# Kernel tuning notes

Hardware: AMD Instinct MI355X
Metric: run time of the kernel (lower is better)

The kernel has to match this reference:

```python
import jax, jax.numpy as jnp
import numpy as np


def _sobel_kernels(dtype):
    # kornia sobel order=1, normalized: divide by sum(|k|)=8
    gx = jnp.array([[-1., 0., 1.], [-2., 0., 2.], [-1., 0., 1.]], dtype=dtype) / 8.0
    gy = gx.T
    return jnp.stack([gx, gy])[:, None]  # (2, 1, 3, 3) OIHW


def _spatial_gradient(x):
    # x: (b, c, h, w) -> gx, gy each (b, c, h, w)
    b, c, h, w = x.shape
    xp = jnp.pad(x.reshape(b * c, 1, h, w), ((0, 0), (0, 0), (1, 1), (1, 1)), mode='edge')
    k = _sobel_kernels(x.dtype)
    out = jax.lax.conv_general_dilated(
        xp, k, window_strides=(1, 1), padding='VALID',
        dimension_numbers=('NCHW', 'OIHW', 'NCHW'))  # (b*c, 2, h, w)
    out = out.reshape(b, c, 2, h, w)
    return out[:, :, 0], out[:, :, 1]


def setup_inputs() -> dict:
    key = jax.random.key(0)
    x = jax.random.normal(key, (16, 3, 512, 512), dtype=jnp.float32)
    return {"x": x}


def reference(x):
    b, c, h, w = x.shape
    gx, gy = _spatial_gradient(x)  # (b, c, h, w) each
    if c == 3:
        mag_c = jnp.sqrt(gx * gx + gy * gy + 1e-9)  # per-channel magnitude
        # first-occurrence argmax over channels matches torch .max(dim) tie-break
        idx = jnp.argmax(mag_c, axis=1)  # (b, h, w)
        gxs = jnp.take_along_axis(gx, idx[:, None], axis=1)[:, 0]  # (b, h, w)
        gys = jnp.take_along_axis(gy, idx[:, None], axis=1)[:, 0]
    else:
        gxs, gys = gx, gy
    magnitude = jnp.sqrt(gxs * gxs + gys * gys + 1e-9)
    # clipped_div(gx, gy, 10.0)
    y_tr = jnp.where(gys == 0.0, jnp.asarray(1e-9, gys.dtype), gys)
    angle = jnp.clip(gxs / y_tr, -10.0, 10.0)
    return magnitude, angle
```

## Files before the change

### kernel.cpp

```cpp
#include <hip/hip_runtime.h>
#include <stdint.h>


constexpr int Hc = 512;
constexpr int Wc = 512;
constexpr int Cc = 3;
constexpr int RT = 4;
constexpr int TR = RT + 2;

__global__ __launch_bounds__(256, 4) void sobel_mag_angle_kernel(
    const float* __restrict__ x, float* __restrict__ out, int B) {
    __shared__ float lds[Cc * TR * Wc];

    int bid = blockIdx.x;
    int b  = bid >> 7;
    int h0 = (bid & 127) * RT;

    int t = threadIdx.x;
    int wave = t >> 6;
    int lane = t & 63;

    const float* xb = x + (size_t)b * (Cc * Hc * Wc);
#pragma unroll
    for (int s2 = 0; s2 < 9; ++s2) {
        int s = wave * 9 + s2;
        int ch = s / 12;
        int rr = (s % 12) >> 1;
        int half = s & 1;
        int srow = h0 + rr - 1;
        srow = srow < 0 ? 0 : (srow > Hc - 1 ? Hc - 1 : srow);
        const float* gp = xb + ((size_t)ch * Hc + srow) * Wc + half * 256 + lane * 4;
        float* lp = &lds[(ch * TR + rr) * Wc + half * 256];
        __builtin_amdgcn_global_load_lds(
            (const __attribute__((address_space(1))) void*)gp,
            (__attribute__((address_space(3))) void*)lp, 16, 0, 0);
    }
    asm volatile("s_waitcnt vmcnt(0)" ::: "memory");
    __syncthreads();

    int r = wave;
    int w0 = lane << 3;
    int wl = (w0 == 0) ? 0 : w0 - 1;
    int wr = (w0 + 8 < Wc) ? w0 + 8 : Wc - 1;

    float bm[8], bgx[8], bgy[8];
#pragma unroll
    for (int c = 0; c < Cc; ++c) {
        float row[3][10];
#pragma unroll
        for (int k = 0; k < 3; ++k) {
            const float* lrow = &lds[(c * TR + (r + k)) * Wc];
            float4 A  = *(const float4*)(lrow + w0);
            float4 Bv = *(const float4*)(lrow + w0 + 4);
            row[k][0] = lrow[wl];
            row[k][1] = A.x;  row[k][2] = A.y;  row[k][3] = A.z;  row[k][4] = A.w;
            row[k][5] = Bv.x; row[k][6] = Bv.y; row[k][7] = Bv.z; row[k][8] = Bv.w;
            row[k][9] = lrow[wr];
        }
#pragma unroll
        for (int i = 0; i < 8; ++i) {
            float t0 = row[0][i + 2] - row[0][i];
            float t1 = row[1][i + 2] - row[1][i];
            float t2 = row[2][i + 2] - row[2][i];
            float gx = 0.125f * (t0 + t2) + 0.25f * t1;
            float u0 = row[2][i]     - row[0][i];
            float u1 = row[2][i + 1] - row[0][i + 1];
            float u2 = row[2][i + 2] - row[0][i + 2];
            float gy = 0.125f * (u0 + u2) + 0.25f * u1;
            float m = __builtin_amdgcn_sqrtf(gx * gx + gy * gy + 1e-9f);
            if (c == 0) {
                bm[i] = m; bgx[i] = gx; bgy[i] = gy;
            } else {
                bool gt = m > bm[i];
                bm[i]  = gt ? m  : bm[i];
                bgx[i] = gt ? gx : bgx[i];
                bgy[i] = gt ? gy : bgy[i];
            }
        }
    }

    float mo[8], ao[8];
#pragma unroll
    for (int i = 0; i < 8; ++i) {
        mo[i] = bm[i];
        float yt = (bgy[i] == 0.0f) ? 1e-9f : bgy[i];
        float a = bgx[i] * __builtin_amdgcn_rcpf(yt);
        ao[i] = fminf(fmaxf(a, -10.0f), 10.0f);
    }

    size_t npix = (size_t)B * (Hc * Wc);
    size_t obase = ((size_t)b * Hc + (h0 + r)) * Wc;
    float* po = out + obase;
    *(float4*)(po + w0)            = make_float4(mo[0], mo[1], mo[2], mo[3]);
    *(float4*)(po + w0 + 4)        = make_float4(mo[4], mo[5], mo[6], mo[7]);
    *(float4*)(po + npix + w0)     = make_float4(ao[0], ao[1], ao[2], ao[3]);
    *(float4*)(po + npix + w0 + 4) = make_float4(ao[4], ao[5], ao[6], ao[7]);
}

extern "C" void kernel_launch(void* const* d_in, const int* in_sizes, int n_in,
                              void* d_out, int out_size, void* d_ws, size_t ws_size,
                              hipStream_t stream) {
    const float* x = (const float*)d_in[0];
    float* out = (float*)d_out;
    int B = in_sizes[0] / (Cc * Hc * Wc);
    int blocks = B * (Hc / RT);
    sobel_mag_angle_kernel<<<blocks, 256, 0, stream>>>(x, out, B);
}
```

Baseline: 96.31 us.

## Make blocks persistent over row strips with triple-buffered async LDS loads

Each block now walks 32 rows in 8 iterations instead of handling one 4-row tile. A 3-slot LDS ring is filled with global_load_lds two stages ahead, and counted vmcnt waits let loads overlap compute. Halo rows are no longer reloaded per tile, and the horizontal halo columns now come from wave shuffles instead of extra LDS reads. The grid shrinks to 256 blocks and LDS use per block grows, which lowers occupancy and may leave too little parallelism to hide memory latency on a GPU with many CUs.

```diff
diff --git a/kernel.cpp b/kernel.cpp
--- a/kernel.cpp
+++ b/kernel.cpp
@@ -6,95 +6,117 @@
 constexpr int Wc = 512;
 constexpr int Cc = 3;
 constexpr int RT = 4;
-constexpr int TR = RT + 2;
+constexpr int ITERS = 8;
+constexpr int SLOTS = 3;
+constexpr int TILE_F = Cc * RT * Wc;
 
-__global__ __launch_bounds__(256, 4) void sobel_mag_angle_kernel(
+__global__ __launch_bounds__(256, 1) void sobel_mag_angle_kernel(
     const float* __restrict__ x, float* __restrict__ out, int B) {
-    __shared__ float lds[Cc * TR * Wc];
+    __shared__ float lds[SLOTS * TILE_F];
 
     int bid = blockIdx.x;
-    int b  = bid >> 7;
-    int h0 = (bid & 127) * RT;
+    int b = bid >> 4;
+    int bstart = (bid & 15) << 5;
 
     int t = threadIdx.x;
     int wave = t >> 6;
     int lane = t & 63;
+    int w0 = lane << 3;
+    bool l0 = (lane == 0), l63 = (lane == 63);
 
     const float* xb = x + (size_t)b * (Cc * Hc * Wc);
+
+    auto stage = [&](int j) {
+        int slot = j % SLOTS;
 #pragma unroll
-    for (int s2 = 0; s2 < 9; ++s2) {
-        int s = wave * 9 + s2;
-        int ch = s / 12;
-        int rr = (s % 12) >> 1;
-        int half = s & 1;
-        int srow = h0 + rr - 1;
-        srow = srow < 0 ? 0 : (srow > Hc - 1 ? Hc - 1 : srow);
-        const float* gp = xb + ((size_t)ch * Hc + srow) * Wc + half * 256 + lane * 4;
-        float* lp = &lds[(ch * TR + rr) * Wc + half * 256];
-        __builtin_amdgcn_global_load_lds(
-            (const __attribute__((address_space(1))) void*)gp,
-            (__attribute__((address_space(3))) void*)lp, 16, 0, 0);
-    }
-    asm volatile("s_waitcnt vmcnt(0)" ::: "memory");
-    __syncthreads();
+        for (int s2 = 0; s2 < 6; ++s2) {
+            int s = wave * 6 + s2;
+            int c = s >> 3;
+            int k = (s >> 1) & 3;
+            int half = s & 1;
+            int g = bstart - 1 + (j << 2) + k;
+            g = g < 0 ? 0 : (g > Hc - 1 ? Hc - 1 : g);
+            const float* gp = xb + ((size_t)c * Hc + g) * Wc + half * 256 + lane * 4;
+            float* lp = &lds[slot * TILE_F + (c * RT + k) * Wc + half * 256];
+            __builtin_amdgcn_global_load_lds(
+                (const __attribute__((address_space(1))) void*)gp,
+                (__attribute__((address_space(3))) void*)lp, 16, 0, 0);
+        }
+    };
 
-    int r = wave;
-    int w0 = lane << 3;
-    int wl = (w0 == 0) ? 0 : w0 - 1;
-    int wr = (w0 + 8 < Wc) ? w0 + 8 : Wc - 1;
+    stage(0);
+    stage(1);
 
-    float bm[8], bgx[8], bgy[8];
+    size_t npix = (size_t)B * (Hc * Wc);
+
+    for (int i = 0; i < ITERS; ++i) {
+        stage(i + 2);
+        asm volatile("s_waitcnt vmcnt(6)" ::: "memory");
+        __builtin_amdgcn_s_barrier();
+        __builtin_amdgcn_sched_barrier(0);
+
+        int si = i % SLOTS, si1 = (i + 1) % SLOTS;
+        float bm[8], bgx[8], bgy[8];
 #pragma unroll
-    for (int c = 0; c < Cc; ++c) {
-        float row[3][10];
+        for (int c = 0; c < Cc; ++c) {
+            float row[3][10];
 #pragma unroll
-        for (int k = 0; k < 3; ++k) {
-            const float* lrow = &lds[(c * TR + (r + k)) * Wc];
-            float4 A  = *(const float4*)(lrow + w0);
-            float4 Bv = *(const float4*)(lrow + w0 + 4);
-            row[k][0] = lrow[wl];
-            row[k][1] = A.x;  row[k][2] = A.y;  row[k][3] = A.z;  row[k][4] = A.w;
-            row[k][5] = Bv.x; row[k][6] = Bv.y; row[k][7] = Bv.z; row[k][8] = Bv.w;
-            row[k][9] = lrow[wr];
-        }
+            for (int d = 0; d < 3; ++d) {
+                int idx = wave + d;
+                int slot = idx < 4 ? si : si1;
+                int k = idx < 4 ? idx : idx - 4;
+                const float* lrow = &lds[slot * TILE_F + (c * RT + k) * Wc];
+                float4 A  = *(const float4*)(lrow + w0);
+                float4 Bv = *(const float4*)(lrow + w0 + 4);
+                float lh = __shfl_up(Bv.w, 1);  lh = l0 ? A.x : lh;
+                float rh = __shfl_down(A.x, 1); rh = l63 ? Bv.w : rh;
+                row[d][0] = lh;
+                row[d][1] = A.x;  row[d][2] = A.y;  row[d][3] = A.z;  row[d][4] = A.w;
+                row[d][5] = Bv.x; row[d][6] = Bv.y; row[d][7] = Bv.z; row[d][8] = Bv.w;
+                row[d][9] = rh;
+            }
 #pragma unroll
-        for (int i = 0; i < 8; ++i) {
-            float t0 = row[0][i + 2] - row[0][i];
-            float t1 = row[1][i + 2] - row[1][i];
-            float t2 = row[2][i + 2] - row[2][i];
-            float gx = 0.125f * (t0 + t2) + 0.25f * t1;
-            float u0 = row[2][i]     - row[0][i];
-            float u1 = row[2][i + 1] - row[0][i + 1];
-            float u2 = row[2][i + 2] - row[0][i + 2];
-            float gy = 0.125f * (u0 + u2) + 0.25f * u1;
-            float m = __builtin_amdgcn_sqrtf(gx * gx + gy * gy + 1e-9f);
-            if (c == 0) {
-                bm[i] = m; bgx[i] = gx; bgy[i] = gy;
-            } else {
-                bool gt = m > bm[i];
-                bm[i]  = gt ? m  : bm[i];
-                bgx[i] = gt ? gx : bgx[i];
-                bgy[i] = gt ? gy : bgy[i];
+            for (int ii = 0; ii < 8; ++ii) {
+                float t0 = row[0][ii + 2] - row[0][ii];
+                float t1 = row[1][ii + 2] - row[1][ii];
+                float t2 = row[2][ii + 2] - row[2][ii];
+                float gx = 0.125f * (t0 + t2) + 0.25f * t1;
+                float u0 = row[2][ii]     - row[0][ii];
+                float u1 = row[2][ii + 1] - row[0][ii + 1];
+                float u2 = row[2][ii + 2] - row[0][ii + 2];
+                float gy = 0.125f * (u0 + u2) + 0.25f * u1;
+                float m = __builtin_amdgcn_sqrtf(gx * gx + gy * gy + 1e-9f);
+                if (c == 0) {
+                    bm[ii] = m; bgx[ii] = gx; bgy[ii] = gy;
+                } else {
+                    bool gt = m > bm[ii];
+                    bm[ii]  = gt ? m  : bm[ii];
+                    bgx[ii] = gt ? gx : bgx[ii];
+                    bgy[ii] = gt ? gy : bgy[ii];
+                }
             }
         }
+
+        float mo[8], ao[8];
+#pragma unroll
+        for (int ii = 0; ii < 8; ++ii) {
+            mo[ii] = bm[ii];
+            float yt = (bgy[ii] == 0.0f) ? 1e-9f : bgy[ii];
+            float a = bgx[ii] * __builtin_amdgcn_rcpf(yt);
+            ao[ii] = fminf(fmaxf(a, -10.0f), 10.0f);
+        }
+
+        int g = bstart + (i << 2) + wave;
+        size_t obase = ((size_t)b * Hc + g) * Wc;
+        float* po = out + obase;
+        *(float4*)(po + w0)            = make_float4(mo[0], mo[1], mo[2], mo[3]);
+        *(float4*)(po + w0 + 4)        = make_float4(mo[4], mo[5], mo[6], mo[7]);
+        *(float4*)(po + npix + w0)     = make_float4(ao[0], ao[1], ao[2], ao[3]);
+        *(float4*)(po + npix + w0 + 4) = make_float4(ao[4], ao[5], ao[6], ao[7]);
+
+        __builtin_amdgcn_sched_barrier(0);
+        __builtin_amdgcn_s_barrier();
     }
-
-    float mo[8], ao[8];
-#pragma unroll
-    for (int i = 0; i < 8; ++i) {
-        mo[i] = bm[i];
-        float yt = (bgy[i] == 0.0f) ? 1e-9f : bgy[i];
-        float a = bgx[i] * __builtin_amdgcn_rcpf(yt);
-        ao[i] = fminf(fmaxf(a, -10.0f), 10.0f);
-    }
-
-    size_t npix = (size_t)B * (Hc * Wc);
-    size_t obase = ((size_t)b * Hc + (h0 + r)) * Wc;
-    float* po = out + obase;
-    *(float4*)(po + w0)            = make_float4(mo[0], mo[1], mo[2], mo[3]);
-    *(float4*)(po + w0 + 4)        = make_float4(mo[4], mo[5], mo[6], mo[7]);
-    *(float4*)(po + npix + w0)     = make_float4(ao[0], ao[1], ao[2], ao[3]);
-    *(float4*)(po + npix + w0 + 4) = make_float4(ao[4], ao[5], ao[6], ao[7]);
 }
 
 extern "C" void kernel_launch(void* const* d_in, const int* in_sizes, int n_in,
@@ -103,6 +125,6 @@
     const float* x = (const float*)d_in[0];
     float* out = (float*)d_out;
     int B = in_sizes[0] / (Cc * Hc * Wc);
-    int blocks = B * (Hc / RT);
+    int blocks = B * (Hc / (RT * ITERS));
     sobel_mag_angle_kernel<<<blocks, 256, 0, stream>>>(x, out, B);
 }
```

After: 103.2 us. +7.1%, slower.
